# Kernel optimization log

Hardware: AMD Instinct MI355X
Metric: run time of the kernel (lower is better)

The kernel has to match this reference:

```python
import jax, jax.numpy as jnp
import numpy as np

D, H, O, E, K = 1024, 4096, 1024, 12, 4
N = 8192


def setup_inputs() -> dict:
    key = jax.random.key(0)
    ks = jax.random.split(key, 7)
    s = 0.02
    return {
        "x": jax.random.normal(ks[0], (N, D), dtype=jnp.float32),
        "gate_w": jax.random.normal(ks[1], (D, E), dtype=jnp.float32) * s,
        "gate_b": jnp.zeros((E,), dtype=jnp.float32),
        "w1": jax.random.normal(ks[2], (E, D, H), dtype=jnp.float32) * s,
        "b1": jnp.zeros((E, H), dtype=jnp.float32),
        "w2": jax.random.normal(ks[3], (E, H, O), dtype=jnp.float32) * s,
        "b2": jnp.zeros((E, O), dtype=jnp.float32),
    }


def reference(x, gate_w, gate_b, w1, b1, w2, b2):
    # Gating: full softmax over all experts, then mask to top-k and renormalize
    scores = x @ gate_w + gate_b                      # [N, E]
    _, topk_idx = jax.lax.top_k(scores, K)            # [N, K]
    mask = jnp.sum(jax.nn.one_hot(topk_idx, E, dtype=scores.dtype), axis=-2)  # [N, E]
    weights = jax.nn.softmax(scores, axis=-1) * mask
    weights = weights / (jnp.sum(weights, axis=-1, keepdims=True) + 1e-8)

    # Dense all-expert MLP (faithful to original: every expert on every token)
    h = jax.nn.relu(jnp.einsum("nd,edh->neh", x, w1) + b1)  # [N, E, H]
    outs = jnp.einsum("neh,eho->neo", h, w2) + b2           # [N, E, O]

    return jnp.einsum("ne,neo->no", weights, outs)          # [N, O]
```

## Files before the change

kernel.cpp:

```cpp
#include <hip/hip_runtime.h>
#include <stdint.h>

#define D_DIM 1024
#define H_DIM 4096
#define O_DIM 1024
#define E_NUM 12
#define TOPK 4
#define N_TOK 8192

#define PAIR_CAP 34304

typedef __bf16 bf16x8 __attribute__((ext_vector_type(8)));
typedef float f32x4 __attribute__((ext_vector_type(4)));
typedef unsigned short u16x8 __attribute__((ext_vector_type(8)));

typedef __attribute__((address_space(3))) unsigned int lds_uint;
typedef __attribute__((address_space(1))) const unsigned int glob_uint;

static __device__ __forceinline__ unsigned short f2b(float f) {
  union { float f; unsigned u; } v; v.f = f;
  unsigned r = v.u + 0x7FFFu + ((v.u >> 16) & 1u);
  return (unsigned short)(r >> 16);
}

static __device__ __forceinline__ void gload16(const void* g, void* l) {
  __builtin_amdgcn_global_load_lds((glob_uint*)g, (lds_uint*)l, 16, 0, 0);
}

__global__ __launch_bounds__(256) void cvt_x_kernel(const float* __restrict__ x,
                                                    unsigned short* __restrict__ xb) {
  int i = blockIdx.x * 256 + threadIdx.x;
  const float4* p = reinterpret_cast<const float4*>(x);
  float4 a = p[2 * i], b = p[2 * i + 1];
  uint4 st;
  st.x = (unsigned)f2b(a.x) | ((unsigned)f2b(a.y) << 16);
  st.y = (unsigned)f2b(a.z) | ((unsigned)f2b(a.w) << 16);
  st.z = (unsigned)f2b(b.x) | ((unsigned)f2b(b.y) << 16);
  st.w = (unsigned)f2b(b.z) | ((unsigned)f2b(b.w) << 16);
  reinterpret_cast<uint4*>(xb)[i] = st;
}

__global__ __launch_bounds__(256) void transpose_cvt_kernel(const float* __restrict__ in,
                                                            unsigned short* __restrict__ out,
                                                            int R, int C) {
  __shared__ float tile[64][33];
  int e = blockIdx.z;
  size_t base = (size_t)e * R * C;
  int c0 = blockIdx.x * 32, r0 = blockIdx.y * 64;
  int tx = threadIdx.x & 31, ty = threadIdx.x >> 5;
#pragma unroll
  for (int i = 0; i < 64; i += 8)
    tile[ty + i][tx] = in[base + (size_t)(r0 + ty + i) * C + (c0 + tx)];
  __syncthreads();
#pragma unroll
  for (int k = 0; k < 4; k++) {
    int c = ty + k * 8;
    unsigned lo = f2b(tile[2 * tx][c]);
    unsigned hi = f2b(tile[2 * tx + 1][c]);
    *reinterpret_cast<unsigned*>(&out[base + (size_t)(c0 + c) * R + r0 + 2 * tx]) =
        lo | (hi << 16);
  }
}

__global__ __launch_bounds__(256) void gwt_kernel(const float* __restrict__ gw,
                                                  float* __restrict__ gwT) {
  int e = blockIdx.x;
#pragma unroll
  for (int i = 0; i < 4; i++) {
    int d = i * 256 + threadIdx.x;
    gwT[e * D_DIM + d] = gw[(size_t)d * E_NUM + e];
  }
}

__global__ __launch_bounds__(256) void gating_kernel(const float* __restrict__ x,
                                                     const float* __restrict__ gwT,
                                                     const float* __restrict__ gb,
                                                     int* __restrict__ tk_e,
                                                     float* __restrict__ tk_w) {
  int wv = (blockIdx.x * 256 + threadIdx.x) >> 6;
  int lane = threadIdx.x & 63;
  int n0 = wv * 4;
  if (n0 >= N_TOK) return;

  const float4* x4 = reinterpret_cast<const float4*>(x);
  const float4* g4 = reinterpret_cast<const float4*>(gwT);

  float acc[4][E_NUM];
#pragma unroll
  for (int t = 0; t < 4; t++)
#pragma unroll
    for (int e = 0; e < E_NUM; e++) acc[t][e] = 0.f;

#pragma unroll
  for (int i = 0; i < 4; i++) {
    float4 xv[4];
#pragma unroll
    for (int t = 0; t < 4; t++) xv[t] = x4[(size_t)(n0 + t) * 256 + i * 64 + lane];
#pragma unroll
    for (int e = 0; e < E_NUM; e++) {
      float4 g = g4[e * 256 + i * 64 + lane];
#pragma unroll
      for (int t = 0; t < 4; t++) {
        acc[t][e] += xv[t].x * g.x + xv[t].y * g.y + xv[t].z * g.z + xv[t].w * g.w;
      }
    }
  }

#pragma unroll
  for (int t = 0; t < 4; t++)
#pragma unroll
    for (int e = 0; e < E_NUM; e++) {
      float v = acc[t][e];
#pragma unroll
      for (int s = 32; s > 0; s >>= 1) v += __shfl_xor(v, s, 64);
      acc[t][e] = v;
    }

#pragma unroll
  for (int t = 0; t < 4; t++) {
    if (lane == t) {
      int n = n0 + t;
      float sc[E_NUM], sm[E_NUM];
      float mx = -1e30f;
#pragma unroll
      for (int e = 0; e < E_NUM; e++) { sc[e] = acc[t][e] + gb[e]; mx = fmaxf(mx, sc[e]); }
      float Z = 0.f;
#pragma unroll
      for (int e = 0; e < E_NUM; e++) { sm[e] = expf(sc[e] - mx); Z += sm[e]; }
      bool used[E_NUM];
#pragma unroll
      for (int e = 0; e < E_NUM; e++) used[e] = false;
      int eid[TOPK]; float p[TOPK]; float wsum = 0.f;
      for (int k = 0; k < TOPK; k++) {
        float best = -1e30f; int bi = 0;
        for (int e = 0; e < E_NUM; e++)
          if (!used[e] && sc[e] > best) { best = sc[e]; bi = e; }
        used[bi] = true; eid[k] = bi; p[k] = sm[bi] / Z; wsum += p[k];
      }
      float inv = 1.f / (wsum + 1e-8f);
      for (int k = 0; k < TOPK; k++) {
        tk_e[n * TOPK + k] = eid[k];
        tk_w[n * TOPK + k] = p[k] * inv;
      }
    }
  }
}

__global__ __launch_bounds__(256) void hist_rank_kernel(const int* __restrict__ tk_e,
                                                        int* __restrict__ lr,
                                                        int* __restrict__ bc) {
  int blk = blockIdx.x, t = threadIdx.x;
  int n = blk * 256 + t;
  int4 te = reinterpret_cast<const int4*>(tk_e)[n];
  int lane = t & 63, w = t >> 6;
  __shared__ int wt[4][E_NUM];
  int r0 = 0, r1 = 0, r2 = 0, r3 = 0;
#pragma unroll
  for (int e = 0; e < E_NUM; e++) {
    int flag = (te.x == e) || (te.y == e) || (te.z == e) || (te.w == e);
    unsigned long long m = __ballot(flag);
    int rw = __popcll(m & ((1ull << lane) - 1ull));
    if (lane == 0) wt[w][e] = __popcll(m);
    if (te.x == e) r0 = rw;
    if (te.y == e) r1 = rw;
    if (te.z == e) r2 = rw;
    if (te.w == e) r3 = rw;
  }
  __syncthreads();
#pragma unroll
  for (int e = 0; e < E_NUM; e++) {
    int base = 0;
#pragma unroll
    for (int w2 = 0; w2 < 4; w2++)
      if (w2 < w) base += wt[w2][e];
    if (te.x == e) r0 += base;
    if (te.y == e) r1 += base;
    if (te.z == e) r2 += base;
    if (te.w == e) r3 += base;
  }
  int4 out; out.x = r0; out.y = r1; out.z = r2; out.w = r3;
  reinterpret_cast<int4*>(lr)[n] = out;
  if (t == 0) {
#pragma unroll
    for (int e = 0; e < E_NUM; e++)
      bc[blk * E_NUM + e] = wt[0][e] + wt[1][e] + wt[2][e] + wt[3][e];
  }
}

__global__ __launch_bounds__(64) void scan2_kernel(const int* __restrict__ bc,
                                                   int* __restrict__ poff,
                                                   int* __restrict__ bb) {
  int t = threadIdx.x;
  __shared__ int cnte[E_NUM];
  __shared__ int spoff[E_NUM + 1];
  if (t < E_NUM) {
    int s = 0;
#pragma unroll
    for (int b = 0; b < 32; b++) s += bc[b * E_NUM + t];
    cnte[t] = s;
  }
  __syncthreads();
  if (t == 0) {
    int off = 0; spoff[0] = 0;
    for (int e = 0; e < E_NUM; e++) {
      off += ((cnte[e] + 127) >> 7) << 7;
      spoff[e + 1] = off;
    }
  }
  __syncthreads();
  if (t < E_NUM + 1) poff[t] = spoff[t];
  if (t < E_NUM) {
    int run = spoff[t];
    for (int b = 0; b < 32; b++) {
      bb[b * E_NUM + t] = run;
      run += bc[b * E_NUM + t];
    }
  }
}

__global__ __launch_bounds__(256) void fill_pairs_kernel(int* __restrict__ pt) {
  int i = blockIdx.x * 256 + threadIdx.x;
  if (i < PAIR_CAP) pt[i] = 0;
}

__global__ __launch_bounds__(256) void scatter2_kernel(const int* __restrict__ tk_e,
                                                       int* __restrict__ lr_ip,
                                                       const int* __restrict__ bb,
                                                       int* __restrict__ pt) {
  int n = blockIdx.x * 256 + threadIdx.x;
  if (n >= N_TOK) return;
  int blk = n >> 8;
  int4 te = reinterpret_cast<const int4*>(tk_e)[n];
  int4 l4 = reinterpret_cast<const int4*>(lr_ip)[n];
  int p0 = bb[blk * E_NUM + te.x] + l4.x;
  int p1 = bb[blk * E_NUM + te.y] + l4.y;
  int p2 = bb[blk * E_NUM + te.z] + l4.z;
  int p3 = bb[blk * E_NUM + te.w] + l4.w;
  pt[p0] = n; pt[p1] = n; pt[p2] = n; pt[p3] = n;
  int4 ip; ip.x = p0; ip.y = p1; ip.z = p2; ip.w = p3;
  reinterpret_cast<int4*>(lr_ip)[n] = ip;
}


__global__ __launch_bounds__(256, 2) void gemm1_kernel(
    const unsigned short* __restrict__ xb,
    const unsigned short* __restrict__ w1t,
    const float* __restrict__ b1,
    const int* __restrict__ pair_token,
    const int* __restrict__ poff,
    unsigned short* __restrict__ hbuf,
    int tile0, int tpc) {
  __shared__ unsigned short As[128 * 32];
  __shared__ unsigned short Bs[128 * 32];
  int cpx = gridDim.x >> 3;
  int f = (blockIdx.x & 7) * cpx + (blockIdx.x >> 3);
  int colb = f & 31;
  int tile = f >> 5;

  int t = tile0 + tile;
  int totTiles = poff[E_NUM] >> 7;
  if (t >= totTiles) return;
  int rowg0 = t << 7;
  int e = 0;
#pragma unroll
  for (int i = 1; i < E_NUM; i++) e += (rowg0 >= poff[i]);

  const int tid = threadIdx.x;
  const int lane = tid & 63, wave = tid >> 6;
  const int wm = wave >> 1, wn = wave & 1;
  const int fr = lane & 15, fgq = lane >> 4;

  const int srow = tid >> 2;
  const int skc = (((tid & 3) ^ ((srow >> 1) & 3)) << 3);
  int tok0 = pair_token[rowg0 + srow];
  int tok1 = pair_token[rowg0 + 64 + srow];
  const unsigned short* a0 = xb + (size_t)tok0 * D_DIM + skc;
  const unsigned short* a1 = xb + (size_t)tok1 * D_DIM + skc;
  int n0 = colb << 7;
  const unsigned short* wb = w1t + (size_t)e * H_DIM * D_DIM;
  const unsigned short* b0p = wb + (size_t)(n0 + srow) * D_DIM + skc;
  const unsigned short* b1p = wb + (size_t)(n0 + 64 + srow) * D_DIM + skc;
  unsigned short* lA0 = &As[tid * 8];
  unsigned short* lA1 = &As[2048 + tid * 8];
  unsigned short* lB0 = &Bs[tid * 8];
  unsigned short* lB1 = &Bs[2048 + tid * 8];

  const int cswz = (fgq ^ ((fr >> 1) & 3)) << 3;
  int aoff[4], boff[4];
#pragma unroll
  for (int mf = 0; mf < 4; mf++) aoff[mf] = (wm * 64 + mf * 16 + fr) * 32 + cswz;
#pragma unroll
  for (int nf = 0; nf < 4; nf++) boff[nf] = (wn * 64 + nf * 16 + fr) * 32 + cswz;

  f32x4 acc[4][4];
#pragma unroll
  for (int i = 0; i < 4; i++)
#pragma unroll
    for (int j = 0; j < 4; j++) acc[i][j] = (f32x4){0.f, 0.f, 0.f, 0.f};

  for (int kt = 0; kt < D_DIM / 32; ++kt) {
    int k0 = kt * 32;
    gload16(a0 + k0, lA0);
    gload16(a1 + k0, lA1);
    gload16(b0p + k0, lB0);
    gload16(b1p + k0, lB1);
    __syncthreads();
    bf16x8 af[4], bq[4];
#pragma unroll
    for (int mf = 0; mf < 4; mf++)
      af[mf] = *reinterpret_cast<const bf16x8*>(&As[aoff[mf]]);
#pragma unroll
    for (int nf = 0; nf < 4; nf++)
      bq[nf] = *reinterpret_cast<const bf16x8*>(&Bs[boff[nf]]);
#pragma unroll
    for (int mf = 0; mf < 4; mf++)
#pragma unroll
      for (int nf = 0; nf < 4; nf++)
        acc[mf][nf] = __builtin_amdgcn_mfma_f32_16x16x32_bf16(af[mf], bq[nf], acc[mf][nf], 0, 0, 0);
    __syncthreads();
  }

  int lrow0 = tile << 7;
#pragma unroll
  for (int nf = 0; nf < 4; nf++) {
    int col = n0 + wn * 64 + nf * 16 + fr;
    float bias = b1[e * H_DIM + col];
#pragma unroll
    for (int mf = 0; mf < 4; mf++) {
      int m = wm * 64 + mf * 16 + fgq * 4;
#pragma unroll
      for (int r = 0; r < 4; r++) {
        float v = fmaxf(acc[mf][nf][r] + bias, 0.f);
        hbuf[(size_t)(lrow0 + m + r) * H_DIM + col] = f2b(v);
      }
    }
  }
}

__global__ __launch_bounds__(256, 2) void gemm2_kernel(
    const unsigned short* __restrict__ hbuf,
    const unsigned short* __restrict__ w2t,
    const float* __restrict__ b2,
    const int* __restrict__ poff,
    unsigned short* __restrict__ youts,
    int tile0, int tpc, int nsplit) {
  __shared__ unsigned short As[128 * 32];
  __shared__ unsigned short Bs[128 * 32];
  int cpx = gridDim.x >> 3;
  int f = (blockIdx.x & 7) * cpx + (blockIdx.x >> 3);
  int colb = f & 7;
  int rest = f >> 3;
  int z = rest % nsplit;
  int tile = rest / nsplit;

  int t = tile0 + tile;
  int totTiles = poff[E_NUM] >> 7;
  if (t >= totTiles) return;
  int rowg0 = t << 7;
  int e = 0;
#pragma unroll
  for (int i = 1; i < E_NUM; i++) e += (rowg0 >= poff[i]);

  const int tid = threadIdx.x;
  const int lane = tid & 63, wave = tid >> 6;
  const int wm = wave >> 1, wn = wave & 1;
  const int fr = lane & 15, fgq = lane >> 4;
  const int kspan = H_DIM / nsplit;
  const int kbase = z * kspan;

  const int srow = tid >> 2;
  const int skc = (((tid & 3) ^ ((srow >> 1) & 3)) << 3);
  int lrowb = tile << 7;
  const unsigned short* a0 = hbuf + (size_t)(lrowb + srow) * H_DIM + kbase + skc;
  const unsigned short* a1 = hbuf + (size_t)(lrowb + 64 + srow) * H_DIM + kbase + skc;
  int n0 = colb << 7;
  const unsigned short* wb = w2t + (size_t)e * O_DIM * H_DIM;
  const unsigned short* b0p = wb + (size_t)(n0 + srow) * H_DIM + kbase + skc;
  const unsigned short* b1p = wb + (size_t)(n0 + 64 + srow) * H_DIM + kbase + skc;
  unsigned short* lA0 = &As[tid * 8];
  unsigned short* lA1 = &As[2048 + tid * 8];
  unsigned short* lB0 = &Bs[tid * 8];
  unsigned short* lB1 = &Bs[2048 + tid * 8];

  const int cswz = (fgq ^ ((fr >> 1) & 3)) << 3;
  int aoff[4], boff[4];
#pragma unroll
  for (int mf = 0; mf < 4; mf++) aoff[mf] = (wm * 64 + mf * 16 + fr) * 32 + cswz;
#pragma unroll
  for (int nf = 0; nf < 4; nf++) boff[nf] = (wn * 64 + nf * 16 + fr) * 32 + cswz;

  f32x4 acc[4][4];
#pragma unroll
  for (int i = 0; i < 4; i++)
#pragma unroll
    for (int j = 0; j < 4; j++) acc[i][j] = (f32x4){0.f, 0.f, 0.f, 0.f};

  for (int kt = 0; kt < kspan / 32; ++kt) {
    int k0 = kt * 32;
    gload16(a0 + k0, lA0);
    gload16(a1 + k0, lA1);
    gload16(b0p + k0, lB0);
    gload16(b1p + k0, lB1);
    __syncthreads();
    bf16x8 af[4], bq[4];
#pragma unroll
    for (int mf = 0; mf < 4; mf++)
      af[mf] = *reinterpret_cast<const bf16x8*>(&As[aoff[mf]]);
#pragma unroll
    for (int nf = 0; nf < 4; nf++)
      bq[nf] = *reinterpret_cast<const bf16x8*>(&Bs[boff[nf]]);
#pragma unroll
    for (int mf = 0; mf < 4; mf++)
#pragma unroll
      for (int nf = 0; nf < 4; nf++)
        acc[mf][nf] = __builtin_amdgcn_mfma_f32_16x16x32_bf16(af[mf], bq[nf], acc[mf][nf], 0, 0, 0);
    __syncthreads();
  }

  size_t ybase = (size_t)z * PAIR_CAP;
#pragma unroll
  for (int nf = 0; nf < 4; nf++) {
    int col = n0 + wn * 64 + nf * 16 + fr;
    float bias = (z == 0) ? b2[e * O_DIM + col] : 0.f;
#pragma unroll
    for (int mf = 0; mf < 4; mf++) {
      int m = wm * 64 + mf * 16 + fgq * 4;
#pragma unroll
      for (int r = 0; r < 4; r++) {
        float v = acc[mf][nf][r] + bias;
        youts[(ybase + rowg0 + m + r) * O_DIM + col] = f2b(v);
      }
    }
  }
}

static __device__ __forceinline__ void acc8(float* a, const unsigned short* y, float wk) {
  u16x8 v = *reinterpret_cast<const u16x8*>(y);
#pragma unroll
  for (int j = 0; j < 8; j++)
    a[j] += wk * __uint_as_float((unsigned)v[j] << 16);
}

__global__ __launch_bounds__(256) void reduce_kernel(const unsigned short* __restrict__ youts,
                                                     const int* __restrict__ ip,
                                                     const float* __restrict__ tk_w,
                                                     float* __restrict__ out,
                                                     int nsplit) {
  int gid = blockIdx.x * 256 + threadIdx.x;
  int n = gid >> 7;
  int c0 = (gid & 127) << 3;
  int4 p = reinterpret_cast<const int4*>(ip)[n];
  float4 w = reinterpret_cast<const float4*>(tk_w)[n];
  const size_t zoff = (size_t)PAIR_CAP * O_DIM;
  float a[8];
#pragma unroll
  for (int j = 0; j < 8; j++) a[j] = 0.f;
  {
    const unsigned short* y = youts + (size_t)p.x * O_DIM + c0;
    acc8(a, y, w.x);
    if (nsplit == 2) acc8(a, y + zoff, w.x);
  }
  {
    const unsigned short* y = youts + (size_t)p.y * O_DIM + c0;
    acc8(a, y, w.y);
    if (nsplit == 2) acc8(a, y + zoff, w.y);
  }
  {
    const unsigned short* y = youts + (size_t)p.z * O_DIM + c0;
    acc8(a, y, w.z);
    if (nsplit == 2) acc8(a, y + zoff, w.z);
  }
  {
    const unsigned short* y = youts + (size_t)p.w * O_DIM + c0;
    acc8(a, y, w.w);
    if (nsplit == 2) acc8(a, y + zoff, w.w);
  }
  float* orow = out + (size_t)n * O_DIM + c0;
  float4 o0; o0.x = a[0]; o0.y = a[1]; o0.z = a[2]; o0.w = a[3];
  float4 o1; o1.x = a[4]; o1.y = a[5]; o1.z = a[6]; o1.w = a[7];
  reinterpret_cast<float4*>(orow)[0] = o0;
  reinterpret_cast<float4*>(orow)[1] = o1;
}

extern "C" void kernel_launch(void* const* d_in, const int* in_sizes, int n_in,
                              void* d_out, int out_size, void* d_ws, size_t ws_size,
                              hipStream_t stream) {
  const float* x  = (const float*)d_in[0];
  const float* gw = (const float*)d_in[1];
  const float* gb = (const float*)d_in[2];
  const float* w1 = (const float*)d_in[3];
  const float* b1 = (const float*)d_in[4];
  const float* w2 = (const float*)d_in[5];
  const float* b2 = (const float*)d_in[6];
  float* out = (float*)d_out;

  char* ws = (char*)d_ws;
  size_t off = 0;
  auto alloc = [&](size_t bytes) -> void* {
    void* p = ws + off;
    off = (off + bytes + 255) & ~(size_t)255;
    return p;
  };
  unsigned short* xb   = (unsigned short*)alloc((size_t)N_TOK * D_DIM * 2);
  unsigned short* w1t  = (unsigned short*)alloc((size_t)E_NUM * H_DIM * D_DIM * 2);
  unsigned short* w2t  = (unsigned short*)alloc((size_t)E_NUM * O_DIM * H_DIM * 2);
  float* gwT  = (float*)alloc((size_t)E_NUM * D_DIM * 4);
  int*   tk_e = (int*)alloc((size_t)N_TOK * TOPK * 4);
  float* tk_w = (float*)alloc((size_t)N_TOK * TOPK * 4);
  int*   lr   = (int*)alloc((size_t)N_TOK * TOPK * 4);
  int*   pt   = (int*)alloc((size_t)PAIR_CAP * 4);
  int*   bc   = (int*)alloc(32 * E_NUM * 4);
  int*   bb   = (int*)alloc(32 * E_NUM * 4);
  int*   poff = (int*)alloc(64);

  const size_t HB134 = (size_t)134 * 128 * H_DIM * 2;
  const size_t HB67  = (size_t)67 * 128 * H_DIM * 2;
  const size_t YO    = (size_t)PAIR_CAP * O_DIM * 2;
  int TPC, NCH, NS;
  if (ws_size >= off + HB134 + 2 * YO + 1024)      { TPC = 134; NCH = 2; NS = 2; }
  else if (ws_size >= off + HB134 + YO + 1024)     { TPC = 134; NCH = 2; NS = 1; }
  else                                             { TPC = 67;  NCH = 4; NS = 1; }
  unsigned short* hbuf  = (unsigned short*)alloc((size_t)TPC * 128 * H_DIM * 2);
  unsigned short* youts = (unsigned short*)alloc((size_t)NS * YO);
  if (off > ws_size) return;

  cvt_x_kernel<<<N_TOK * D_DIM / 8 / 256, 256, 0, stream>>>(x, xb);
  transpose_cvt_kernel<<<dim3(H_DIM / 32, D_DIM / 64, E_NUM), 256, 0, stream>>>(w1, w1t, D_DIM, H_DIM);
  transpose_cvt_kernel<<<dim3(O_DIM / 32, H_DIM / 64, E_NUM), 256, 0, stream>>>(w2, w2t, H_DIM, O_DIM);
  gwt_kernel<<<E_NUM, 256, 0, stream>>>(gw, gwT);
  gating_kernel<<<N_TOK / 16, 256, 0, stream>>>(x, gwT, gb, tk_e, tk_w);
  hist_rank_kernel<<<N_TOK / 256, 256, 0, stream>>>(tk_e, lr, bc);
  scan2_kernel<<<1, 64, 0, stream>>>(bc, poff, bb);
  fill_pairs_kernel<<<(PAIR_CAP + 255) / 256, 256, 0, stream>>>(pt);
  scatter2_kernel<<<N_TOK / 256, 256, 0, stream>>>(tk_e, lr, bb, pt);

  for (int c = 0; c < NCH; c++) {
    int tile0 = c * TPC;
    gemm1_kernel<<<dim3((H_DIM / 128) * TPC), 256, 0, stream>>>(xb, w1t, b1, pt, poff, hbuf, tile0, TPC);
    gemm2_kernel<<<dim3((O_DIM / 128) * TPC * NS), 256, 0, stream>>>(hbuf, w2t, b2, poff, youts, tile0, TPC, NS);
  }
  reduce_kernel<<<N_TOK * (O_DIM / 8) / 256, 256, 0, stream>>>(youts, lr, tk_w, out, NS);
}
```

Baseline: 983.1 us.

## Enlarge expert GEMM tiles to 256x256 with double-buffered LDS and phased MFMA scheduling

```diff
diff --git a/kernel.cpp b/kernel.cpp
--- a/kernel.cpp
+++ b/kernel.cpp
@@ -8,7 +8,7 @@
 #define TOPK 4
 #define N_TOK 8192
 
-#define PAIR_CAP 34304
+#define PAIR_CAP 36096
 
 typedef __bf16 bf16x8 __attribute__((ext_vector_type(8)));
 typedef float f32x4 __attribute__((ext_vector_type(4)));
@@ -100,9 +100,8 @@
     for (int e = 0; e < E_NUM; e++) {
       float4 g = g4[e * 256 + i * 64 + lane];
 #pragma unroll
-      for (int t = 0; t < 4; t++) {
+      for (int t = 0; t < 4; t++)
         acc[t][e] += xv[t].x * g.x + xv[t].y * g.y + xv[t].z * g.z + xv[t].w * g.w;
-      }
     }
   }
 
@@ -203,7 +202,7 @@
   if (t == 0) {
     int off = 0; spoff[0] = 0;
     for (int e = 0; e < E_NUM; e++) {
-      off += ((cnte[e] + 127) >> 7) << 7;
+      off += ((cnte[e] + 255) >> 8) << 8;
       spoff[e + 1] = off;
     }
   }
@@ -242,195 +241,227 @@
 }
 
 
-__global__ __launch_bounds__(256, 2) void gemm1_kernel(
+#define PHASE(MF0, EXTRA)                                                          \
+  {                                                                                \
+    bf16x8 af0k0 = *reinterpret_cast<const bf16x8*>(&Asl[((MF0) * 16 + fr) * 64 + aq0e]);     \
+    bf16x8 af0k1 = *reinterpret_cast<const bf16x8*>(&Asl[((MF0) * 16 + fr) * 64 + aq1e]);     \
+    bf16x8 af1k0 = *reinterpret_cast<const bf16x8*>(&Asl[((MF0) * 16 + 16 + fr) * 64 + aq0e]); \
+    bf16x8 af1k1 = *reinterpret_cast<const bf16x8*>(&Asl[((MF0) * 16 + 16 + fr) * 64 + aq1e]); \
+    EXTRA                                                                          \
+    __builtin_amdgcn_s_barrier();                                                  \
+    __builtin_amdgcn_s_setprio(1);                                                 \
+    _Pragma("unroll")                                                              \
+    for (int nf = 0; nf < 4; nf++) {                                               \
+      acc[MF0][nf]     = __builtin_amdgcn_mfma_f32_16x16x32_bf16(af0k0, bfr[nf][0], acc[MF0][nf], 0, 0, 0);     \
+      acc[MF0][nf]     = __builtin_amdgcn_mfma_f32_16x16x32_bf16(af0k1, bfr[nf][1], acc[MF0][nf], 0, 0, 0);     \
+      acc[MF0 + 1][nf] = __builtin_amdgcn_mfma_f32_16x16x32_bf16(af1k0, bfr[nf][0], acc[MF0 + 1][nf], 0, 0, 0); \
+      acc[MF0 + 1][nf] = __builtin_amdgcn_mfma_f32_16x16x32_bf16(af1k1, bfr[nf][1], acc[MF0 + 1][nf], 0, 0, 0); \
+    }                                                                              \
+    __builtin_amdgcn_s_setprio(0);                                                 \
+  }
+
+#define STAGE_A(sb, ko)                                       \
+  gload16(aptr00 + (ko), &Ah[sb][0][tid * 8]);                \
+  gload16(aptr01 + (ko), &Ah[sb][0][4096 + tid * 8]);         \
+  gload16(aptr10 + (ko), &Ah[sb][1][tid * 8]);                \
+  gload16(aptr11 + (ko), &Ah[sb][1][4096 + tid * 8]);
+#define STAGE_B(sb, ko)                                       \
+  gload16(bptr00 + (ko), &Bh[sb][0][tid * 8]);                \
+  gload16(bptr01 + (ko), &Bh[sb][0][4096 + tid * 8]);         \
+  gload16(bptr10 + (ko), &Bh[sb][1][tid * 8]);                \
+  gload16(bptr11 + (ko), &Bh[sb][1][4096 + tid * 8]);
+
+__global__ __launch_bounds__(512, 2) void gemm1_kernel(
     const unsigned short* __restrict__ xb,
     const unsigned short* __restrict__ w1t,
     const float* __restrict__ b1,
     const int* __restrict__ pair_token,
     const int* __restrict__ poff,
     unsigned short* __restrict__ hbuf,
-    int tile0, int tpc) {
-  __shared__ unsigned short As[128 * 32];
-  __shared__ unsigned short Bs[128 * 32];
+    int tile0) {
+  __shared__ unsigned short Ah[2][2][8192];
+  __shared__ unsigned short Bh[2][2][8192];
+
   int cpx = gridDim.x >> 3;
   int f = (blockIdx.x & 7) * cpx + (blockIdx.x >> 3);
-  int colb = f & 31;
-  int tile = f >> 5;
-
+  int colb = f & 15;
+  int tile = f >> 4;
   int t = tile0 + tile;
-  int totTiles = poff[E_NUM] >> 7;
+  int totTiles = poff[E_NUM] >> 8;
   if (t >= totTiles) return;
-  int rowg0 = t << 7;
+  int rowg0 = t << 8;
   int e = 0;
 #pragma unroll
   for (int i = 1; i < E_NUM; i++) e += (rowg0 >= poff[i]);
 
   const int tid = threadIdx.x;
   const int lane = tid & 63, wave = tid >> 6;
-  const int wm = wave >> 1, wn = wave & 1;
+  const int wm = wave >> 2, wn = wave & 3;
   const int fr = lane & 15, fgq = lane >> 4;
-
-  const int srow = tid >> 2;
-  const int skc = (((tid & 3) ^ ((srow >> 1) & 3)) << 3);
-  int tok0 = pair_token[rowg0 + srow];
-  int tok1 = pair_token[rowg0 + 64 + srow];
-  const unsigned short* a0 = xb + (size_t)tok0 * D_DIM + skc;
-  const unsigned short* a1 = xb + (size_t)tok1 * D_DIM + skc;
-  int n0 = colb << 7;
-  const unsigned short* wb = w1t + (size_t)e * H_DIM * D_DIM;
-  const unsigned short* b0p = wb + (size_t)(n0 + srow) * D_DIM + skc;
-  const unsigned short* b1p = wb + (size_t)(n0 + 64 + srow) * D_DIM + skc;
-  unsigned short* lA0 = &As[tid * 8];
-  unsigned short* lA1 = &As[2048 + tid * 8];
-  unsigned short* lB0 = &Bs[tid * 8];
-  unsigned short* lB1 = &Bs[2048 + tid * 8];
-
-  const int cswz = (fgq ^ ((fr >> 1) & 3)) << 3;
-  int aoff[4], boff[4];
-#pragma unroll
-  for (int mf = 0; mf < 4; mf++) aoff[mf] = (wm * 64 + mf * 16 + fr) * 32 + cswz;
-#pragma unroll
-  for (int nf = 0; nf < 4; nf++) boff[nf] = (wn * 64 + nf * 16 + fr) * 32 + cswz;
-
-  f32x4 acc[4][4];
-#pragma unroll
-  for (int i = 0; i < 4; i++)
+  const int frq = fr & 7;
+  const int aq0e = (fgq ^ frq) << 3;
+  const int aq1e = ((4 | fgq) ^ frq) << 3;
+  const int brow = (wn & 1) << 6;
+
+  const int srow = tid >> 3;
+  const int cs = ((tid & 7) ^ (srow & 7)) << 3;
+
+  const unsigned short* aptr00 = xb + (size_t)pair_token[rowg0 + srow] * D_DIM + cs;
+  const unsigned short* aptr01 = xb + (size_t)pair_token[rowg0 + 64 + srow] * D_DIM + cs;
+  const unsigned short* aptr10 = xb + (size_t)pair_token[rowg0 + 128 + srow] * D_DIM + cs;
+  const unsigned short* aptr11 = xb + (size_t)pair_token[rowg0 + 192 + srow] * D_DIM + cs;
+  int n0 = colb << 8;
+  const unsigned short* wbb = w1t + (size_t)e * H_DIM * D_DIM;
+  const unsigned short* bptr00 = wbb + (size_t)(n0 + srow) * D_DIM + cs;
+  const unsigned short* bptr01 = wbb + (size_t)(n0 + 64 + srow) * D_DIM + cs;
+  const unsigned short* bptr10 = wbb + (size_t)(n0 + 128 + srow) * D_DIM + cs;
+  const unsigned short* bptr11 = wbb + (size_t)(n0 + 192 + srow) * D_DIM + cs;
+
+  f32x4 acc[8][4];
+#pragma unroll
+  for (int i = 0; i < 8; i++)
 #pragma unroll
     for (int j = 0; j < 4; j++) acc[i][j] = (f32x4){0.f, 0.f, 0.f, 0.f};
 
-  for (int kt = 0; kt < D_DIM / 32; ++kt) {
-    int k0 = kt * 32;
-    gload16(a0 + k0, lA0);
-    gload16(a1 + k0, lA1);
-    gload16(b0p + k0, lB0);
-    gload16(b1p + k0, lB1);
+  STAGE_A(0, 0);
+  STAGE_B(0, 0);
+  for (int kt = 0; kt < D_DIM / 64; ++kt) {
+    const int s = kt & 1;
+    const int kon = (kt + 1) << 6;
+    const unsigned short* Asl = Ah[s][wm];
+    const unsigned short* Bsl = Bh[s][wn >> 1];
     __syncthreads();
-    bf16x8 af[4], bq[4];
-#pragma unroll
-    for (int mf = 0; mf < 4; mf++)
-      af[mf] = *reinterpret_cast<const bf16x8*>(&As[aoff[mf]]);
-#pragma unroll
-    for (int nf = 0; nf < 4; nf++)
-      bq[nf] = *reinterpret_cast<const bf16x8*>(&Bs[boff[nf]]);
-#pragma unroll
-    for (int mf = 0; mf < 4; mf++)
-#pragma unroll
-      for (int nf = 0; nf < 4; nf++)
-        acc[mf][nf] = __builtin_amdgcn_mfma_f32_16x16x32_bf16(af[mf], bq[nf], acc[mf][nf], 0, 0, 0);
-    __syncthreads();
-  }
-
-  int lrow0 = tile << 7;
+    bf16x8 bfr[4][2];
+#pragma unroll
+    for (int nf = 0; nf < 4; nf++) {
+      bfr[nf][0] = *reinterpret_cast<const bf16x8*>(&Bsl[(brow + nf * 16 + fr) * 64 + aq0e]);
+      bfr[nf][1] = *reinterpret_cast<const bf16x8*>(&Bsl[(brow + nf * 16 + fr) * 64 + aq1e]);
+    }
+    if (kt + 1 < D_DIM / 64) {
+      PHASE(0, STAGE_A(s ^ 1, kon));
+      __builtin_amdgcn_s_barrier();
+      PHASE(2, STAGE_B(s ^ 1, kon));
+    } else {
+      PHASE(0, );
+      __builtin_amdgcn_s_barrier();
+      PHASE(2, );
+    }
+    __builtin_amdgcn_s_barrier();
+    PHASE(4, );
+    __builtin_amdgcn_s_barrier();
+    PHASE(6, );
+  }
+
+  int lrow0 = (tile << 8) + (wm << 7);
 #pragma unroll
   for (int nf = 0; nf < 4; nf++) {
     int col = n0 + wn * 64 + nf * 16 + fr;
     float bias = b1[e * H_DIM + col];
 #pragma unroll
-    for (int mf = 0; mf < 4; mf++) {
-      int m = wm * 64 + mf * 16 + fgq * 4;
+    for (int mf = 0; mf < 8; mf++)
 #pragma unroll
       for (int r = 0; r < 4; r++) {
         float v = fmaxf(acc[mf][nf][r] + bias, 0.f);
-        hbuf[(size_t)(lrow0 + m + r) * H_DIM + col] = f2b(v);
+        hbuf[(size_t)(lrow0 + mf * 16 + fgq * 4 + r) * H_DIM + col] = f2b(v);
       }
-    }
-  }
-}
-
-__global__ __launch_bounds__(256, 2) void gemm2_kernel(
+  }
+}
+
+__global__ __launch_bounds__(512, 2) void gemm2_kernel(
     const unsigned short* __restrict__ hbuf,
     const unsigned short* __restrict__ w2t,
     const float* __restrict__ b2,
     const int* __restrict__ poff,
     unsigned short* __restrict__ youts,
-    int tile0, int tpc, int nsplit) {
-  __shared__ unsigned short As[128 * 32];
-  __shared__ unsigned short Bs[128 * 32];
+    int tile0) {
+  __shared__ unsigned short Ah[2][2][8192];
+  __shared__ unsigned short Bh[2][2][8192];
+
   int cpx = gridDim.x >> 3;
   int f = (blockIdx.x & 7) * cpx + (blockIdx.x >> 3);
-  int colb = f & 7;
-  int rest = f >> 3;
-  int z = rest % nsplit;
-  int tile = rest / nsplit;
-
+  int colb = f & 3;
+  int z = (f >> 2) & 1;
+  int tile = f >> 3;
   int t = tile0 + tile;
-  int totTiles = poff[E_NUM] >> 7;
+  int totTiles = poff[E_NUM] >> 8;
   if (t >= totTiles) return;
-  int rowg0 = t << 7;
+  int rowg0 = t << 8;
   int e = 0;
 #pragma unroll
   for (int i = 1; i < E_NUM; i++) e += (rowg0 >= poff[i]);
 
   const int tid = threadIdx.x;
   const int lane = tid & 63, wave = tid >> 6;
-  const int wm = wave >> 1, wn = wave & 1;
+  const int wm = wave >> 2, wn = wave & 3;
   const int fr = lane & 15, fgq = lane >> 4;
-  const int kspan = H_DIM / nsplit;
-  const int kbase = z * kspan;
-
-  const int srow = tid >> 2;
-  const int skc = (((tid & 3) ^ ((srow >> 1) & 3)) << 3);
-  int lrowb = tile << 7;
-  const unsigned short* a0 = hbuf + (size_t)(lrowb + srow) * H_DIM + kbase + skc;
-  const unsigned short* a1 = hbuf + (size_t)(lrowb + 64 + srow) * H_DIM + kbase + skc;
-  int n0 = colb << 7;
-  const unsigned short* wb = w2t + (size_t)e * O_DIM * H_DIM;
-  const unsigned short* b0p = wb + (size_t)(n0 + srow) * H_DIM + kbase + skc;
-  const unsigned short* b1p = wb + (size_t)(n0 + 64 + srow) * H_DIM + kbase + skc;
-  unsigned short* lA0 = &As[tid * 8];
-  unsigned short* lA1 = &As[2048 + tid * 8];
-  unsigned short* lB0 = &Bs[tid * 8];
-  unsigned short* lB1 = &Bs[2048 + tid * 8];
-
-  const int cswz = (fgq ^ ((fr >> 1) & 3)) << 3;
-  int aoff[4], boff[4];
-#pragma unroll
-  for (int mf = 0; mf < 4; mf++) aoff[mf] = (wm * 64 + mf * 16 + fr) * 32 + cswz;
-#pragma unroll
-  for (int nf = 0; nf < 4; nf++) boff[nf] = (wn * 64 + nf * 16 + fr) * 32 + cswz;
-
-  f32x4 acc[4][4];
-#pragma unroll
-  for (int i = 0; i < 4; i++)
+  const int frq = fr & 7;
+  const int aq0e = (fgq ^ frq) << 3;
+  const int aq1e = ((4 | fgq) ^ frq) << 3;
+  const int brow = (wn & 1) << 6;
+
+  const int srow = tid >> 3;
+  const int cs = ((tid & 7) ^ (srow & 7)) << 3;
+  const int kbase = z << 11;
+
+  int lrowb = tile << 8;
+  const unsigned short* aptr00 = hbuf + (size_t)(lrowb + srow) * H_DIM + kbase + cs;
+  const unsigned short* aptr01 = hbuf + (size_t)(lrowb + 64 + srow) * H_DIM + kbase + cs;
+  const unsigned short* aptr10 = hbuf + (size_t)(lrowb + 128 + srow) * H_DIM + kbase + cs;
+  const unsigned short* aptr11 = hbuf + (size_t)(lrowb + 192 + srow) * H_DIM + kbase + cs;
+  int n0 = colb << 8;
+  const unsigned short* wbb = w2t + (size_t)e * O_DIM * H_DIM;
+  const unsigned short* bptr00 = wbb + (size_t)(n0 + srow) * H_DIM + kbase + cs;
+  const unsigned short* bptr01 = wbb + (size_t)(n0 + 64 + srow) * H_DIM + kbase + cs;
+  const unsigned short* bptr10 = wbb + (size_t)(n0 + 128 + srow) * H_DIM + kbase + cs;
+  const unsigned short* bptr11 = wbb + (size_t)(n0 + 192 + srow) * H_DIM + kbase + cs;
+
+  f32x4 acc[8][4];
+#pragma unroll
+  for (int i = 0; i < 8; i++)
 #pragma unroll
     for (int j = 0; j < 4; j++) acc[i][j] = (f32x4){0.f, 0.f, 0.f, 0.f};
 
-  for (int kt = 0; kt < kspan / 32; ++kt) {
-    int k0 = kt * 32;
-    gload16(a0 + k0, lA0);
-    gload16(a1 + k0, lA1);
-    gload16(b0p + k0, lB0);
-    gload16(b1p + k0, lB1);
+  STAGE_A(0, 0);
+  STAGE_B(0, 0);
+  for (int kt = 0; kt < 32; ++kt) {
+    const int s = kt & 1;
+    const int kon = (kt + 1) << 6;
+    const unsigned short* Asl = Ah[s][wm];
+    const unsigned short* Bsl = Bh[s][wn >> 1];
     __syncthreads();
-    bf16x8 af[4], bq[4];
-#pragma unroll
-    for (int mf = 0; mf < 4; mf++)
-      af[mf] = *reinterpret_cast<const bf16x8*>(&As[aoff[mf]]);
-#pragma unroll
-    for (int nf = 0; nf < 4; nf++)
-      bq[nf] = *reinterpret_cast<const bf16x8*>(&Bs[boff[nf]]);
-#pragma unroll
-    for (int mf = 0; mf < 4; mf++)
-#pragma unroll
-      for (int nf = 0; nf < 4; nf++)
-        acc[mf][nf] = __builtin_amdgcn_mfma_f32_16x16x32_bf16(af[mf], bq[nf], acc[mf][nf], 0, 0, 0);
-    __syncthreads();
-  }
-
-  size_t ybase = (size_t)z * PAIR_CAP;
+    bf16x8 bfr[4][2];
+#pragma unroll
+    for (int nf = 0; nf < 4; nf++) {
+      bfr[nf][0] = *reinterpret_cast<const bf16x8*>(&Bsl[(brow + nf * 16 + fr) * 64 + aq0e]);
+      bfr[nf][1] = *reinterpret_cast<const bf16x8*>(&Bsl[(brow + nf * 16 + fr) * 64 + aq1e]);
+    }
+    if (kt + 1 < 32) {
+      PHASE(0, STAGE_A(s ^ 1, kon));
+      __builtin_amdgcn_s_barrier();
+      PHASE(2, STAGE_B(s ^ 1, kon));
+    } else {
+      PHASE(0, );
+      __builtin_amdgcn_s_barrier();
+      PHASE(2, );
+    }
+    __builtin_amdgcn_s_barrier();
+    PHASE(4, );
+    __builtin_amdgcn_s_barrier();
+    PHASE(6, );
+  }
+
+  size_t ybase = (size_t)z * PAIR_CAP + rowg0 + (wm << 7);
 #pragma unroll
   for (int nf = 0; nf < 4; nf++) {
     int col = n0 + wn * 64 + nf * 16 + fr;
     float bias = (z == 0) ? b2[e * O_DIM + col] : 0.f;
 #pragma unroll
-    for (int mf = 0; mf < 4; mf++) {
-      int m = wm * 64 + mf * 16 + fgq * 4;
+    for (int mf = 0; mf < 8; mf++)
 #pragma unroll
       for (int r = 0; r < 4; r++) {
         float v = acc[mf][nf][r] + bias;
-        youts[(ybase + rowg0 + m + r) * O_DIM + col] = f2b(v);
+        youts[(ybase + mf * 16 + fgq * 4 + r) * O_DIM + col] = f2b(v);
       }
-    }
   }
 }
 
@@ -444,8 +475,7 @@
 __global__ __launch_bounds__(256) void reduce_kernel(const unsigned short* __restrict__ youts,
                                                      const int* __restrict__ ip,
                                                      const float* __restrict__ tk_w,
-                                                     float* __restrict__ out,
-                                                     int nsplit) {
+                                                     float* __restrict__ out) {
   int gid = blockIdx.x * 256 + threadIdx.x;
   int n = gid >> 7;
   int c0 = (gid & 127) << 3;
@@ -457,23 +487,19 @@
   for (int j = 0; j < 8; j++) a[j] = 0.f;
   {
     const unsigned short* y = youts + (size_t)p.x * O_DIM + c0;
-    acc8(a, y, w.x);
-    if (nsplit == 2) acc8(a, y + zoff, w.x);
+    acc8(a, y, w.x); acc8(a, y + zoff, w.x);
   }
   {
     const unsigned short* y = youts + (size_t)p.y * O_DIM + c0;
-    acc8(a, y, w.y);
-    if (nsplit == 2) acc8(a, y + zoff, w.y);
+    acc8(a, y, w.y); acc8(a, y + zoff, w.y);
   }
   {
     const unsigned short* y = youts + (size_t)p.z * O_DIM + c0;
-    acc8(a, y, w.z);
-    if (nsplit == 2) acc8(a, y + zoff, w.z);
+    acc8(a, y, w.z); acc8(a, y + zoff, w.z);
   }
   {
     const unsigned short* y = youts + (size_t)p.w * O_DIM + c0;
-    acc8(a, y, w.w);
-    if (nsplit == 2) acc8(a, y + zoff, w.w);
+    acc8(a, y, w.w); acc8(a, y + zoff, w.w);
   }
   float* orow = out + (size_t)n * O_DIM + c0;
   float4 o0; o0.x = a[0]; o0.y = a[1]; o0.z = a[2]; o0.w = a[3];
@@ -513,15 +539,16 @@
   int*   bb   = (int*)alloc(32 * E_NUM * 4);
   int*   poff = (int*)alloc(64);
 
-  const size_t HB134 = (size_t)134 * 128 * H_DIM * 2;
-  const size_t HB67  = (size_t)67 * 128 * H_DIM * 2;
-  const size_t YO    = (size_t)PAIR_CAP * O_DIM * 2;
-  int TPC, NCH, NS;
-  if (ws_size >= off + HB134 + 2 * YO + 1024)      { TPC = 134; NCH = 2; NS = 2; }
-  else if (ws_size >= off + HB134 + YO + 1024)     { TPC = 134; NCH = 2; NS = 1; }
-  else                                             { TPC = 67;  NCH = 4; NS = 1; }
-  unsigned short* hbuf  = (unsigned short*)alloc((size_t)TPC * 128 * H_DIM * 2);
-  unsigned short* youts = (unsigned short*)alloc((size_t)NS * YO);
+  const size_t YO2 = (size_t)2 * PAIR_CAP * O_DIM * 2;
+  auto need = [&](int tpcN) {
+    return off + (size_t)tpcN * 256 * H_DIM * 2 + YO2 + 2048;
+  };
+  int TPC, NCH;
+  if (ws_size >= need(141))      { TPC = 141; NCH = 1; }
+  else if (ws_size >= need(71))  { TPC = 71;  NCH = 2; }
+  else                           { TPC = 47;  NCH = 3; }
+  unsigned short* hbuf  = (unsigned short*)alloc((size_t)TPC * 256 * H_DIM * 2);
+  unsigned short* youts = (unsigned short*)alloc(YO2);
   if (off > ws_size) return;
 
   cvt_x_kernel<<<N_TOK * D_DIM / 8 / 256, 256, 0, stream>>>(x, xb);
@@ -536,8 +563,8 @@
 
   for (int c = 0; c < NCH; c++) {
     int tile0 = c * TPC;
-    gemm1_kernel<<<dim3((H_DIM / 128) * TPC), 256, 0, stream>>>(xb, w1t, b1, pt, poff, hbuf, tile0, TPC);
-    gemm2_kernel<<<dim3((O_DIM / 128) * TPC * NS), 256, 0, stream>>>(hbuf, w2t, b2, poff, youts, tile0, TPC, NS);
-  }
-  reduce_kernel<<<N_TOK * (O_DIM / 8) / 256, 256, 0, stream>>>(youts, lr, tk_w, out, NS);
-}
+    gemm1_kernel<<<dim3(16 * TPC), 512, 0, stream>>>(xb, w1t, b1, pt, poff, hbuf, tile0);
+    gemm2_kernel<<<dim3(8 * TPC), 512, 0, stream>>>(hbuf, w2t, b2, poff, youts, tile0);
+  }
+  reduce_kernel<<<N_TOK * (O_DIM / 8) / 256, 256, 0, stream>>>(youts, lr, tk_w, out);
+}
```

Measured after the change: 996.8 us. Within noise of the previous version (+1.4%).
